# Kernel optimization log

Hardware: AMD Instinct MI355X
Metric: run time of the kernel (lower is better)

The kernel has to match this reference:

```python
import jax, jax.numpy as jnp
import numpy as np

RX = (2, 9)
RY = (4, 9)
G, O = 64, 2          # column chunk size and overlap (hardcoded in original forward)
GK = RX[1]            # Gaussian (uniform box) kernel size, must be odd
M = N = 512


def _patches(x, kh, kw, pc, pr):
    # torch: F.pad(x,(pr,pr,pc,pc)).unfold(-2,kh,1).unfold(-2,kw,1).flatten(-2)
    xp = jnp.pad(x, ((0, 0), (0, 0), (pc, pc), (pr, pr)))
    p = jax.lax.conv_general_dilated_patches(xp, (kh, kw), (1, 1), 'VALID')  # (b, kh*kw, m, n) since c==1
    return jnp.moveaxis(p, 1, -1)[:, None]  # (b,1,m,n,kh*kw)


def _spatial_kernel(kh, kw):
    d = (jnp.arange(kh, dtype=jnp.float32) - kh // 2)[:, None] ** 2 \
        + (jnp.arange(kw, dtype=jnp.float32) - kw // 2)[None, :] ** 2
    return jnp.exp(-d.reshape(-1) / ((kh * kw) / 4.0) ** 2)


def _gen_weight(ych, kh, kw, pc, pr, sigma):
    p = _patches(ych, kh, kw, pc, pr)
    w = jnp.exp(-((p - ych[..., None]) ** 2) / (sigma / 2.0) ** 2)  # range (bilateral) term
    w = w * _spatial_kernel(kh, kw)                                  # spatial Gaussian term
    w = w * _patches(jnp.ones_like(ych), kh, kw, pc, pr)             # zero out padded taps
    return w / w.sum(-1, keepdims=True)


def _boxfilter(x, weight, kh, kw, pc, pr):
    return (_patches(x, kh, kw, pc, pr) * weight).sum(-1)


def _forward(X, y, r):
    sigma = r[0] * (y.max() - y.min())
    kh0, kw0, pc0, pr0 = 2 * RX[0] + 1, 2 * RY[0] + 1, RX[0], RY[0]  # detail kernel
    kh1, kw1, pc1, pr1 = 2 * RX[1] + 1, 2 * RY[1] + 1, RX[1], RY[1]  # base kernel
    gk = jnp.ones((1, 1, GK, GK), X.dtype) / float(GK * GK)
    pad = GK // 2
    conv = lambda z: jax.lax.conv_general_dilated(z, gk, (1, 1), [(pad, pad), (pad, pad)])

    # Angle = [0]: rotate(.,0,expand=True) and CenterCrop(m,n) are identities.
    XX, yy = X, y
    XXbase, yybase = conv(XX), conv(yy)
    XXdetail, yydetail = XX - XXbase, yy - yybase

    n = X.shape[-1]
    idx = np.arange(n)
    chunks = [idx[i:i + G] for i in range(0, n, G - O)]
    if len(chunks[-1]) <= 5:
        chunks[-2] = np.arange(chunks[-2][0], n)
        del chunks[-1]

    bdetail, Abase, bbase = [], [], []
    for index, ck in enumerate(chunks):
        s, e = int(ck[0]), int(ck[-1]) + 1
        Xb, Xd = XXbase[..., s:e], XXdetail[..., s:e]
        yb, yd = yybase[..., s:e], yydetail[..., s:e]
        wD = _gen_weight(Xd, kh0, kw0, pc0, pr0, sigma)
        wB = _gen_weight(Xb, kh1, kw1, pc1, pr1, sigma)
        lo = 0 if index == 0 else O // 2
        hi = None if index == len(chunks) - 1 else -(O // 2)
        bdetail.append(_boxfilter(yd - Xd, wD, kh0, kw0, pc0, pr0)[..., lo:hi])
        mean_y = _boxfilter(yb, wB, kh1, kw1, pc1, pr1)
        mean_x = _boxfilter(Xb, wB, kh1, kw1, pc1, pr1)
        var_x = _boxfilter(Xb * Xb, wB, kh1, kw1, pc1, pr1) - mean_x * mean_x
        cov_xy = _boxfilter(Xb * yb, wB, kh1, kw1, pc1, pr1) - mean_x * mean_y
        A = cov_xy / (var_x + 1e-6)
        b = mean_y - A * mean_x
        bbase.append(b[..., lo:hi])
        Abase.append(A[..., lo:hi])

    bdetail = jnp.concatenate(bdetail, -1)
    Abase = jnp.concatenate(Abase, -1)
    bbase = jnp.concatenate(bbase, -1)
    return Abase * XXbase + bbase + XXdetail + bdetail


def setup_inputs() -> dict:
    key = jax.random.key(0)
    k1, k2, k3 = jax.random.split(key, 3)
    X = jax.random.uniform(k1, (1, 1, M, N), dtype=jnp.float32)
    y = jax.random.uniform(k2, (1, 1, M, N), dtype=jnp.float32)
    r = jax.random.uniform(k3, (1,), dtype=jnp.float32)
    return {"X": X, "y": y, "r": r}


def reference(X, y, r):
    return _forward(X, y, r)
```

## Files before the change

kernel.cpp:

```cpp
#include <hip/hip_runtime.h>

#define W 512
#define NPIX (512*512)

__global__ __launch_bounds__(256) void k_reduce(const float* __restrict__ y,
                                                float* __restrict__ partial) {
    __shared__ float smn[256], smx[256];
    int t = threadIdx.x;
    int base = blockIdx.x * 1024 + t;
    float mn = 1e30f, mx = -1e30f;
#pragma unroll
    for (int k = 0; k < 4; ++k) {
        float v = y[base + k * 256];
        mn = fminf(mn, v);
        mx = fmaxf(mx, v);
    }
    smn[t] = mn; smx[t] = mx;
    __syncthreads();
    for (int off = 128; off > 0; off >>= 1) {
        if (t < off) {
            smn[t] = fminf(smn[t], smn[t + off]);
            smx[t] = fmaxf(smx[t], smx[t + off]);
        }
        __syncthreads();
    }
    if (t == 0) {
        partial[blockIdx.x]       = smn[0];
        partial[256 + blockIdx.x] = smx[0];
    }
}

__global__ __launch_bounds__(256) void k_sigma(const float* __restrict__ partial,
                                               const float* __restrict__ r,
                                               float* __restrict__ k2out) {
    __shared__ float smn[256], smx[256];
    int t = threadIdx.x;
    smn[t] = partial[t];
    smx[t] = partial[256 + t];
    __syncthreads();
    for (int off = 128; off > 0; off >>= 1) {
        if (t < off) {
            smn[t] = fminf(smn[t], smn[t + off]);
            smx[t] = fmaxf(smx[t], smx[t + off]);
        }
        __syncthreads();
    }
    if (t == 0) {
        float sigma = r[0] * (smx[0] - smn[0]);
        float hh = 0.5f * sigma;
        k2out[0] = -1.4426950408889634f / (hh * hh);
    }
}

__device__ __forceinline__ float fexp2(float x) {
#if __has_builtin(__builtin_amdgcn_exp2f)
    return __builtin_amdgcn_exp2f(x);
#else
    return __expf(x * 0.6931471805599453f);
#endif
}

__global__ __launch_bounds__(256) void k_row(const float* __restrict__ X,
                                             const float* __restrict__ y,
                                             float* __restrict__ tmpX,
                                             float* __restrict__ tmpY) {
    __shared__ float sX[4][80], sY[4][80];
    int tx = threadIdx.x, ty = threadIdx.y;
    int c0 = blockIdx.x * 64;
    int h  = blockIdx.y * 4 + ty;
    {
        int col = c0 - 4 + tx;
        sX[ty][tx] = ((unsigned)col < 512u) ? X[h * W + col] : 0.f;
        sY[ty][tx] = ((unsigned)col < 512u) ? y[h * W + col] : 0.f;
        if (tx < 8) {
            int col2 = c0 + 60 + tx;
            sX[ty][64 + tx] = ((unsigned)col2 < 512u) ? X[h * W + col2] : 0.f;
            sY[ty][64 + tx] = ((unsigned)col2 < 512u) ? y[h * W + col2] : 0.f;
        }
    }
    __syncthreads();
    float sx = 0.f, sy = 0.f;
#pragma unroll
    for (int j = 0; j < 9; ++j) {
        sx += sX[ty][tx + j];
        sy += sY[ty][tx + j];
    }
    int c = c0 + tx;
    tmpX[h * W + c] = sx;
    tmpY[h * W + c] = sy;
}

__global__ __launch_bounds__(256) void k_col(const float* __restrict__ X,
                                             const float* __restrict__ y,
                                             const float* __restrict__ tmpX,
                                             const float* __restrict__ tmpY,
                                             float* __restrict__ Xb,
                                             float* __restrict__ yb,
                                             float* __restrict__ Xd,
                                             float* __restrict__ Dd) {
    int c = blockIdx.x * 64 + threadIdx.x;
    int h = blockIdx.y * 4 + threadIdx.y;
    float sx = 0.f, sy = 0.f;
#pragma unroll
    for (int dy = -4; dy <= 4; ++dy) {
        int nh = h + dy;
        if ((unsigned)nh < 512u) {
            sx += tmpX[nh * W + c];
            sy += tmpY[nh * W + c];
        }
    }
    const float inv81 = 1.0f / 81.0f;
    float xbv = sx * inv81, ybv = sy * inv81;
    int p = h * W + c;
    float xv = X[p], yv = y[p];
    float xd = xv - xbv;
    Xb[p] = xbv;
    yb[p] = ybv;
    Xd[p] = xd;
    Dd[p] = (yv - ybv) - xd;
}

__global__ __launch_bounds__(256) void k_main(const float* __restrict__ Xb,
                                              const float* __restrict__ yb,
                                              const float* __restrict__ Xd,
                                              const float* __restrict__ Dd,
                                              const float* __restrict__ k2p,
                                              float* __restrict__ out) {
    __shared__ float sbx[19];
    __shared__ float sdx[9];
    __shared__ float sdy[5];
    int t = threadIdx.y * 64 + threadIdx.x;
    if (t < 19) { int d = t - 9; sbx[t] = __expf(-(float)(d * d) / 8145.0625f); }
    else if (t < 32) { int u = t - 19; if (u < 9)  { int d = u - 4; sdx[u] = __expf(-(float)(d * d) / 126.5625f); } }
    else if (t < 40) { int u = t - 32; if (u < 5)  { int d = u - 2; sdy[u] = __expf(-(float)(d * d) / 126.5625f); } }
    __syncthreads();

    float k2 = k2p[0];
    int c = blockIdx.x * 64 + threadIdx.x;
    int h = blockIdx.y * 4 + threadIdx.y;

    int chunk = (c == 0) ? 0 : (c - 1) / 62;
    if (chunk > 8) chunk = 8;
    int s = 62 * chunk;
    int e = (chunk == 8) ? 512 : (s + 64);

    float colw[19];
#pragma unroll
    for (int j = 0; j < 19; ++j) {
        int nc = c - 9 + j;
        colw[j] = ((nc >= s) & (nc < e)) ? sbx[j] : 0.f;
    }
    float colwd[9];
#pragma unroll
    for (int j = 0; j < 9; ++j) {
        int nc = c - 4 + j;
        colwd[j] = ((nc >= s) & (nc < e)) ? sdx[j] : 0.f;
    }

    int p = h * W + c;
    float Xc  = Xb[p];
    float Xdc = Xd[p];

    float sw = 0.f, swy = 0.f, swx = 0.f, swxx = 0.f, swxy = 0.f;
#pragma unroll 1
    for (int dy = -9; dy <= 9; ++dy) {
        int nh = h + dy;
        if ((unsigned)nh >= 512u) continue;
        const float* xr = Xb + nh * W + c;
        const float* yr = yb + nh * W + c;
        float ey = sbx[dy + 9];
        float rs = 0.f, rsx = 0.f, rsy = 0.f, rsxx = 0.f, rsxy = 0.f;
#pragma unroll
        for (int j = 0; j < 19; ++j) {
            float xv = xr[j - 9];
            float yv = yr[j - 9];
            float dd = xv - Xc;
            float w  = fexp2(dd * (dd * k2)) * colw[j];
            float tt = w * xv;
            rs   += w;
            rsx  += tt;
            rsy  = fmaf(w, yv, rsy);
            rsxx = fmaf(tt, xv, rsxx);
            rsxy = fmaf(tt, yv, rsxy);
        }
        sw   = fmaf(ey, rs,   sw);
        swx  = fmaf(ey, rsx,  swx);
        swy  = fmaf(ey, rsy,  swy);
        swxx = fmaf(ey, rsxx, swxx);
        swxy = fmaf(ey, rsxy, swxy);
    }

    float swd = 0.f, sv = 0.f;
#pragma unroll 1
    for (int dy = -2; dy <= 2; ++dy) {
        int nh = h + dy;
        if ((unsigned)nh >= 512u) continue;
        const float* xr = Xd + nh * W + c;
        const float* dr = Dd + nh * W + c;
        float ey = sdy[dy + 2];
        float rs = 0.f, rv = 0.f;
#pragma unroll
        for (int j = 0; j < 9; ++j) {
            float xd = xr[j - 4];
            float dv = dr[j - 4];
            float dd = xd - Xdc;
            float w  = fexp2(dd * (dd * k2)) * colwd[j];
            rs += w;
            rv  = fmaf(w, dv, rv);
        }
        swd = fmaf(ey, rs, swd);
        sv  = fmaf(ey, rv, sv);
    }

    float inv_sw = 1.0f / sw;
    float mx = swx * inv_sw, my = swy * inv_sw;
    float varx = fmaf(-mx, mx, swxx * inv_sw);
    float cov  = fmaf(-mx, my, swxy * inv_sw);
    float A = cov / (varx + 1e-6f);
    float b = my - A * mx;
    out[p] = A * Xc + b + Xdc + sv / swd;
}

extern "C" void kernel_launch(void* const* d_in, const int* in_sizes, int n_in,
                              void* d_out, int out_size, void* d_ws, size_t ws_size,
                              hipStream_t stream) {
    const float* X = (const float*)d_in[0];
    const float* y = (const float*)d_in[1];
    const float* r = (const float*)d_in[2];
    float* out = (float*)d_out;
    float* wsf = (float*)d_ws;

    const int GA = 256;
    float* k2      = wsf;
    float* partial = wsf + 64;
    float* tmpX = wsf + 1024 + GA;
    float* tmpY = tmpX + NPIX + 2 * GA;
    float* Xb   = tmpY + NPIX + 2 * GA;
    float* yb   = Xb   + NPIX + 2 * GA;
    float* Xd   = yb   + NPIX + 2 * GA;
    float* Dd   = Xd   + NPIX + 2 * GA;

    k_reduce<<<256, 256, 0, stream>>>(y, partial);
    k_sigma<<<1, 256, 0, stream>>>(partial, r, k2);
    k_row<<<dim3(8, 128), dim3(64, 4), 0, stream>>>(X, y, tmpX, tmpY);
    k_col<<<dim3(8, 128), dim3(64, 4), 0, stream>>>(X, y, tmpX, tmpY, Xb, yb, Xd, Dd);
    k_main<<<dim3(8, 128), dim3(64, 4), 0, stream>>>(Xb, yb, Xd, Dd, k2, out);
}
```

Measured before the change: 109.4 us.

## Fuse prep kernels, interleave planes as float2, and compute two rows per thread

Merges the sigma reduction, row box filter and column box filter into one k_prep kernel that does the separable 9x9 box sum in shared memory. The base and detail planes are stored interleaved as float2 so each neighbour tap takes one 8-byte load. The main bilateral kernel now has each thread produce two vertically adjacent output rows, sharing every neighbour load between both, with 128-thread blocks. This cuts launches, intermediate global traffic and redundant loads, at the cost of more registers per thread and fewer threads in flight.

Result: faster. 103.0 us (-5.8%).

```diff
diff --git a/kernel.cpp b/kernel.cpp
--- a/kernel.cpp
+++ b/kernel.cpp
@@ -30,28 +30,6 @@
     }
 }
 
-__global__ __launch_bounds__(256) void k_sigma(const float* __restrict__ partial,
-                                               const float* __restrict__ r,
-                                               float* __restrict__ k2out) {
-    __shared__ float smn[256], smx[256];
-    int t = threadIdx.x;
-    smn[t] = partial[t];
-    smx[t] = partial[256 + t];
-    __syncthreads();
-    for (int off = 128; off > 0; off >>= 1) {
-        if (t < off) {
-            smn[t] = fminf(smn[t], smn[t + off]);
-            smx[t] = fmaxf(smx[t], smx[t + off]);
-        }
-        __syncthreads();
-    }
-    if (t == 0) {
-        float sigma = r[0] * (smx[0] - smn[0]);
-        float hh = 0.5f * sigma;
-        k2out[0] = -1.4426950408889634f / (hh * hh);
-    }
-}
-
 __device__ __forceinline__ float fexp2(float x) {
 #if __has_builtin(__builtin_amdgcn_exp2f)
     return __builtin_amdgcn_exp2f(x);
@@ -60,84 +38,79 @@
 #endif
 }
 
-__global__ __launch_bounds__(256) void k_row(const float* __restrict__ X,
-                                             const float* __restrict__ y,
-                                             float* __restrict__ tmpX,
-                                             float* __restrict__ tmpY) {
-    __shared__ float sX[4][80], sY[4][80];
+__global__ __launch_bounds__(512) void k_prep(const float* __restrict__ X,
+                                              const float* __restrict__ y,
+                                              const float* __restrict__ partial,
+                                              const float* __restrict__ r,
+                                              float2* __restrict__ XYb,
+                                              float2* __restrict__ XDd,
+                                              float* __restrict__ k2out) {
     int tx = threadIdx.x, ty = threadIdx.y;
-    int c0 = blockIdx.x * 64;
-    int h  = blockIdx.y * 4 + ty;
-    {
-        int col = c0 - 4 + tx;
-        sX[ty][tx] = ((unsigned)col < 512u) ? X[h * W + col] : 0.f;
-        sY[ty][tx] = ((unsigned)col < 512u) ? y[h * W + col] : 0.f;
-        if (tx < 8) {
-            int col2 = c0 + 60 + tx;
-            sX[ty][64 + tx] = ((unsigned)col2 < 512u) ? X[h * W + col2] : 0.f;
-            sY[ty][64 + tx] = ((unsigned)col2 < 512u) ? y[h * W + col2] : 0.f;
-        }
-    }
-    __syncthreads();
-    float sx = 0.f, sy = 0.f;
-#pragma unroll
-    for (int j = 0; j < 9; ++j) {
-        sx += sX[ty][tx + j];
-        sy += sY[ty][tx + j];
-    }
-    int c = c0 + tx;
-    tmpX[h * W + c] = sx;
-    tmpY[h * W + c] = sy;
-}
-
-__global__ __launch_bounds__(256) void k_col(const float* __restrict__ X,
-                                             const float* __restrict__ y,
-                                             const float* __restrict__ tmpX,
-                                             const float* __restrict__ tmpY,
-                                             float* __restrict__ Xb,
-                                             float* __restrict__ yb,
-                                             float* __restrict__ Xd,
-                                             float* __restrict__ Dd) {
-    int c = blockIdx.x * 64 + threadIdx.x;
-    int h = blockIdx.y * 4 + threadIdx.y;
-    float sx = 0.f, sy = 0.f;
-#pragma unroll
-    for (int dy = -4; dy <= 4; ++dy) {
-        int nh = h + dy;
-        if ((unsigned)nh < 512u) {
-            sx += tmpX[nh * W + c];
-            sy += tmpY[nh * W + c];
-        }
-    }
+    int t = ty * 64 + tx;
+    if (blockIdx.y == 64) {
+        if (blockIdx.x != 0) return;
+        __shared__ float smn[256], smx[256];
+        if (t < 256) { smn[t] = partial[t]; smx[t] = partial[256 + t]; }
+        __syncthreads();
+        for (int off = 128; off > 0; off >>= 1) {
+            if (t < off) { smn[t] = fminf(smn[t], smn[t + off]); smx[t] = fmaxf(smx[t], smx[t + off]); }
+            __syncthreads();
+        }
+        if (t == 0) {
+            float sigma = r[0] * (smx[0] - smn[0]);
+            float hh = 0.5f * sigma;
+            k2out[0] = -1.4426950408889634f / (hh * hh);
+        }
+        return;
+    }
+    __shared__ float sX[16][72], sY[16][72];
+    __shared__ float rX[16][64], rY[16][64];
+    int c0 = blockIdx.x * 64, r0 = blockIdx.y * 8;
+    for (int i = t; i < 16 * 72; i += 512) {
+        int rr = i / 72, cc = i - rr * 72;
+        int gr = r0 - 4 + rr, gc = c0 - 4 + cc;
+        bool ok = ((unsigned)gr < 512u) & ((unsigned)gc < 512u);
+        sX[rr][cc] = ok ? X[gr * W + gc] : 0.f;
+        sY[rr][cc] = ok ? y[gr * W + gc] : 0.f;
+    }
+    __syncthreads();
+    for (int i = t; i < 16 * 64; i += 512) {
+        int rr = i >> 6, cc = i & 63;
+        float ax = 0.f, ay = 0.f;
+#pragma unroll
+        for (int j = 0; j < 9; ++j) { ax += sX[rr][cc + j]; ay += sY[rr][cc + j]; }
+        rX[rr][cc] = ax; rY[rr][cc] = ay;
+    }
+    __syncthreads();
+    float ax = 0.f, ay = 0.f;
+#pragma unroll
+    for (int j = 0; j < 9; ++j) { ax += rX[ty + j][tx]; ay += rY[ty + j][tx]; }
     const float inv81 = 1.0f / 81.0f;
-    float xbv = sx * inv81, ybv = sy * inv81;
-    int p = h * W + c;
-    float xv = X[p], yv = y[p];
-    float xd = xv - xbv;
-    Xb[p] = xbv;
-    yb[p] = ybv;
-    Xd[p] = xd;
-    Dd[p] = (yv - ybv) - xd;
-}
-
-__global__ __launch_bounds__(256) void k_main(const float* __restrict__ Xb,
-                                              const float* __restrict__ yb,
-                                              const float* __restrict__ Xd,
-                                              const float* __restrict__ Dd,
+    float xb = ax * inv81, yb = ay * inv81;
+    float xv = sX[ty + 4][tx + 4], yv = sY[ty + 4][tx + 4];
+    float xd = xv - xb;
+    int p = (r0 + ty) * W + (c0 + tx);
+    XYb[p] = make_float2(xb, yb);
+    XDd[p] = make_float2(xd, (yv - yb) - xd);
+}
+
+__global__ __launch_bounds__(128) void k_main(const float2* __restrict__ XYb,
+                                              const float2* __restrict__ XDd,
                                               const float* __restrict__ k2p,
                                               float* __restrict__ out) {
     __shared__ float sbx[19];
     __shared__ float sdx[9];
     __shared__ float sdy[5];
-    int t = threadIdx.y * 64 + threadIdx.x;
-    if (t < 19) { int d = t - 9; sbx[t] = __expf(-(float)(d * d) / 8145.0625f); }
-    else if (t < 32) { int u = t - 19; if (u < 9)  { int d = u - 4; sdx[u] = __expf(-(float)(d * d) / 126.5625f); } }
-    else if (t < 40) { int u = t - 32; if (u < 5)  { int d = u - 2; sdy[u] = __expf(-(float)(d * d) / 126.5625f); } }
+    int tx = threadIdx.x, ty = threadIdx.y;
+    int t = ty * 64 + tx;
+    if (t < 19)      { int d = t - 9;      sbx[t]      = __expf(-(float)(d * d) / 8145.0625f); }
+    else if (t < 28) { int d = t - 19 - 4; sdx[t - 19] = __expf(-(float)(d * d) / 126.5625f); }
+    else if (t < 33) { int d = t - 28 - 2; sdy[t - 28] = __expf(-(float)(d * d) / 126.5625f); }
     __syncthreads();
 
     float k2 = k2p[0];
-    int c = blockIdx.x * 64 + threadIdx.x;
-    int h = blockIdx.y * 4 + threadIdx.y;
+    int c  = blockIdx.x * 64 + tx;
+    int h0 = (blockIdx.y * 2 + ty) * 2;
 
     int chunk = (c == 0) ? 0 : (c - 1) / 62;
     if (chunk > 8) chunk = 8;
@@ -157,68 +130,87 @@
         colwd[j] = ((nc >= s) & (nc < e)) ? sdx[j] : 0.f;
     }
 
-    int p = h * W + c;
-    float Xc  = Xb[p];
-    float Xdc = Xd[p];
-
-    float sw = 0.f, swy = 0.f, swx = 0.f, swxx = 0.f, swxy = 0.f;
+    int p0 = h0 * W + c;
+    float Xc0  = XYb[p0].x,     Xc1  = XYb[p0 + W].x;
+    float2 cd0 = XDd[p0];
+    float2 cd1 = XDd[p0 + W];
+    float Xd0 = cd0.x, Xd1 = cd1.x;
+
+    float sw0 = 0.f, swx0 = 0.f, swy0 = 0.f, swxx0 = 0.f, swxy0 = 0.f;
+    float sw1 = 0.f, swx1 = 0.f, swy1 = 0.f, swxx1 = 0.f, swxy1 = 0.f;
 #pragma unroll 1
-    for (int dy = -9; dy <= 9; ++dy) {
-        int nh = h + dy;
+    for (int nh = h0 - 9; nh <= h0 + 10; ++nh) {
         if ((unsigned)nh >= 512u) continue;
-        const float* xr = Xb + nh * W + c;
-        const float* yr = yb + nh * W + c;
-        float ey = sbx[dy + 9];
-        float rs = 0.f, rsx = 0.f, rsy = 0.f, rsxx = 0.f, rsxy = 0.f;
+        int dy0 = nh - h0;
+        const float2* xr = XYb + (nh * W + c);
+        float rs0 = 0.f, rsx0 = 0.f, rsy0 = 0.f, rsxx0 = 0.f, rsxy0 = 0.f;
+        float rs1 = 0.f, rsx1 = 0.f, rsy1 = 0.f, rsxx1 = 0.f, rsxy1 = 0.f;
 #pragma unroll
         for (int j = 0; j < 19; ++j) {
-            float xv = xr[j - 9];
-            float yv = yr[j - 9];
-            float dd = xv - Xc;
-            float w  = fexp2(dd * (dd * k2)) * colw[j];
-            float tt = w * xv;
-            rs   += w;
-            rsx  += tt;
-            rsy  = fmaf(w, yv, rsy);
-            rsxx = fmaf(tt, xv, rsxx);
-            rsxy = fmaf(tt, yv, rsxy);
-        }
-        sw   = fmaf(ey, rs,   sw);
-        swx  = fmaf(ey, rsx,  swx);
-        swy  = fmaf(ey, rsy,  swy);
-        swxx = fmaf(ey, rsxx, swxx);
-        swxy = fmaf(ey, rsxy, swxy);
-    }
-
-    float swd = 0.f, sv = 0.f;
+            float2 v = xr[j - 9];
+            float xv = v.x, yv = v.y;
+            float u0 = xv - Xc0,        u1 = xv - Xc1;
+            float a0 = u0 * (u0 * k2),  a1 = u1 * (u1 * k2);
+            float w0 = fexp2(a0) * colw[j];
+            float w1 = fexp2(a1) * colw[j];
+            rs0 += w0;                      rs1 += w1;
+            rsx0 = fmaf(w0, xv, rsx0);      rsx1 = fmaf(w1, xv, rsx1);
+            rsy0 = fmaf(w0, yv, rsy0);      rsy1 = fmaf(w1, yv, rsy1);
+            float t0 = w0 * xv,             t1 = w1 * xv;
+            rsxx0 = fmaf(t0, xv, rsxx0);    rsxx1 = fmaf(t1, xv, rsxx1);
+            rsxy0 = fmaf(t0, yv, rsxy0);    rsxy1 = fmaf(t1, yv, rsxy1);
+        }
+        float ey0 = (dy0 <= 9)  ? sbx[dy0 + 9] : 0.f;
+        float ey1 = (dy0 >= -8) ? sbx[dy0 + 8] : 0.f;
+        sw0   = fmaf(ey0, rs0,   sw0);    sw1   = fmaf(ey1, rs1,   sw1);
+        swx0  = fmaf(ey0, rsx0,  swx0);   swx1  = fmaf(ey1, rsx1,  swx1);
+        swy0  = fmaf(ey0, rsy0,  swy0);   swy1  = fmaf(ey1, rsy1,  swy1);
+        swxx0 = fmaf(ey0, rsxx0, swxx0);  swxx1 = fmaf(ey1, rsxx1, swxx1);
+        swxy0 = fmaf(ey0, rsxy0, swxy0);  swxy1 = fmaf(ey1, rsxy1, swxy1);
+    }
+
+    float swd0 = 0.f, sv0 = 0.f, swd1 = 0.f, sv1 = 0.f;
 #pragma unroll 1
-    for (int dy = -2; dy <= 2; ++dy) {
-        int nh = h + dy;
+    for (int nh = h0 - 2; nh <= h0 + 3; ++nh) {
         if ((unsigned)nh >= 512u) continue;
-        const float* xr = Xd + nh * W + c;
-        const float* dr = Dd + nh * W + c;
-        float ey = sdy[dy + 2];
-        float rs = 0.f, rv = 0.f;
+        int dyd = nh - h0;
+        const float2* dr = XDd + (nh * W + c);
+        float rs0 = 0.f, rv0 = 0.f, rs1 = 0.f, rv1 = 0.f;
 #pragma unroll
         for (int j = 0; j < 9; ++j) {
-            float xd = xr[j - 4];
-            float dv = dr[j - 4];
-            float dd = xd - Xdc;
-            float w  = fexp2(dd * (dd * k2)) * colwd[j];
-            rs += w;
-            rv  = fmaf(w, dv, rv);
-        }
-        swd = fmaf(ey, rs, swd);
-        sv  = fmaf(ey, rv, sv);
-    }
-
-    float inv_sw = 1.0f / sw;
-    float mx = swx * inv_sw, my = swy * inv_sw;
-    float varx = fmaf(-mx, mx, swxx * inv_sw);
-    float cov  = fmaf(-mx, my, swxy * inv_sw);
-    float A = cov / (varx + 1e-6f);
-    float b = my - A * mx;
-    out[p] = A * Xc + b + Xdc + sv / swd;
+            float2 v = dr[j - 4];
+            float xd = v.x, dv = v.y;
+            float u0 = xd - Xd0,        u1 = xd - Xd1;
+            float a0 = u0 * (u0 * k2),  a1 = u1 * (u1 * k2);
+            float w0 = fexp2(a0) * colwd[j];
+            float w1 = fexp2(a1) * colwd[j];
+            rs0 += w0;                  rs1 += w1;
+            rv0 = fmaf(w0, dv, rv0);    rv1 = fmaf(w1, dv, rv1);
+        }
+        float ey0 = (dyd <= 2)  ? sdy[dyd + 2] : 0.f;
+        float ey1 = (dyd >= -1) ? sdy[dyd + 1] : 0.f;
+        swd0 = fmaf(ey0, rs0, swd0);  swd1 = fmaf(ey1, rs1, swd1);
+        sv0  = fmaf(ey0, rv0, sv0);   sv1  = fmaf(ey1, rv1, sv1);
+    }
+
+    {
+        float inv = 1.0f / sw0;
+        float mx = swx0 * inv, my = swy0 * inv;
+        float varx = fmaf(-mx, mx, swxx0 * inv);
+        float cov  = fmaf(-mx, my, swxy0 * inv);
+        float A = cov / (varx + 1e-6f);
+        float b = my - A * mx;
+        out[p0] = A * Xc0 + b + Xd0 + sv0 / swd0;
+    }
+    {
+        float inv = 1.0f / sw1;
+        float mx = swx1 * inv, my = swy1 * inv;
+        float varx = fmaf(-mx, mx, swxx1 * inv);
+        float cov  = fmaf(-mx, my, swxy1 * inv);
+        float A = cov / (varx + 1e-6f);
+        float b = my - A * mx;
+        out[p0 + W] = A * Xc1 + b + Xd1 + sv1 / swd1;
+    }
 }
 
 extern "C" void kernel_launch(void* const* d_in, const int* in_sizes, int n_in,
@@ -230,19 +222,12 @@
     float* out = (float*)d_out;
     float* wsf = (float*)d_ws;
 
-    const int GA = 256;
     float* k2      = wsf;
     float* partial = wsf + 64;
-    float* tmpX = wsf + 1024 + GA;
-    float* tmpY = tmpX + NPIX + 2 * GA;
-    float* Xb   = tmpY + NPIX + 2 * GA;
-    float* yb   = Xb   + NPIX + 2 * GA;
-    float* Xd   = yb   + NPIX + 2 * GA;
-    float* Dd   = Xd   + NPIX + 2 * GA;
+    float2* XYb = (float2*)(wsf + 1024) + 256;
+    float2* XDd = XYb + NPIX + 512;
 
     k_reduce<<<256, 256, 0, stream>>>(y, partial);
-    k_sigma<<<1, 256, 0, stream>>>(partial, r, k2);
-    k_row<<<dim3(8, 128), dim3(64, 4), 0, stream>>>(X, y, tmpX, tmpY);
-    k_col<<<dim3(8, 128), dim3(64, 4), 0, stream>>>(X, y, tmpX, tmpY, Xb, yb, Xd, Dd);
-    k_main<<<dim3(8, 128), dim3(64, 4), 0, stream>>>(Xb, yb, Xd, Dd, k2, out);
-}
+    k_prep<<<dim3(8, 65), dim3(64, 8), 0, stream>>>(X, y, partial, r, XYb, XDd, k2);
+    k_main<<<dim3(8, 128), dim3(64, 2), 0, stream>>>(XYb, XDd, k2, out);
+}
```
